# Kernel tuning notes

Hardware: AMD Instinct MI355X
Metric: run time of the kernel (lower is better)

Reference implementation:

```python
import jax, jax.numpy as jnp
import numpy as np

HEADS = 4
KDIM = 512
HALF = KDIM // 2
KNN = 16
NKEYS = 512
INPUT_DIM = 1024
VDIM = 512
B, T = 2, 1024


def setup_inputs() -> dict:
    key = jax.random.key(0)
    ks = jax.random.split(key, 5)
    bound_k = 1.0 / np.sqrt(KDIM)
    x = jax.random.normal(ks[0], (B, T, INPUT_DIM), dtype=jnp.float32)
    Wq = jax.random.normal(ks[1], (HEADS * KDIM, INPUT_DIM), dtype=jnp.float32) * (1.0 / np.sqrt(INPUT_DIM))
    bq = jnp.zeros((HEADS * KDIM,), dtype=jnp.float32)
    keys = jax.random.uniform(ks[2], (2 * HEADS * NKEYS, HALF), dtype=jnp.float32, minval=-bound_k, maxval=bound_k)
    values = jax.random.normal(ks[3], (NKEYS * NKEYS, VDIM), dtype=jnp.float32) * (VDIM ** -0.5)
    return {"x": x, "Wq": Wq, "bq": bq, "keys": keys, "values": values}


def reference(x, Wq, bq, keys, values):
    Bb, Tt, C = x.shape
    bs = Bb * Tt
    x_flat = x.reshape(bs, C)
    # query projection -> (bs, heads, k_dim)
    q = (x_flat @ Wq.T + bq).reshape(bs, HEADS, KDIM)
    q1, q2 = q[..., :HALF], q[..., HALF:]
    kk = keys.reshape(HEADS, 2, NKEYS, HALF)
    k1, k2 = kk[:, 0], kk[:, 1]
    # subspace scores: (bs, heads, n_keys)
    s1 = jnp.einsum('blh,lkh->blk', q1, k1)
    s2 = jnp.einsum('blh,lkh->blk', q2, k2)
    s1, i1 = jax.lax.top_k(s1, KNN)
    s2, i2 = jax.lax.top_k(s2, KNN)
    # cartesian merge -> (bs, heads, knn*knn)
    all_s = (s1[:, :, :, None] + s2[:, :, None, :]).reshape(bs, HEADS, KNN * KNN)
    all_i = (i1[:, :, :, None] * NKEYS + i2[:, :, None, :]).reshape(bs, HEADS, KNN * KNN)
    s, best = jax.lax.top_k(all_s, KNN)
    idx = jnp.take_along_axis(all_i, best, axis=2)  # (bs, heads, knn)
    # softmax per (token, head) over knn, in fp32 (matches torch F.softmax on (bs*heads, knn))
    w = jax.nn.softmax(s.astype(jnp.float32), axis=-1)
    idx_f = idx.reshape(bs, HEADS * KNN)
    w_f = w.reshape(bs, HEADS * KNN)
    # embedding_bag mode='sum' with per-sample weights
    out = jnp.einsum('bk,bkd->bd', w_f, values[idx_f].astype(jnp.float32))
    return out.reshape(Bb, Tt, VDIM).astype(x.dtype)
```

## Files before the change

kernel.cpp:

```cpp
#include <hip/hip_runtime.h>

typedef __attribute__((ext_vector_type(8))) _Float16 half8;
typedef __attribute__((ext_vector_type(8)))  short   short8;
typedef __attribute__((ext_vector_type(4)))  float   floatx4;
typedef __attribute__((ext_vector_type(2)))  float   floatx2;
typedef unsigned short ushort;

__device__ __forceinline__ void gl_lds16(const void* g, void* lds) {
    __builtin_amdgcn_global_load_lds(
        (const __attribute__((address_space(1))) unsigned int*)g,
        (__attribute__((address_space(3))) unsigned int*)lds,
        16, 0, 0);
}

__global__ void split2_kernel(const float* __restrict__ src,
                              _Float16* __restrict__ ph,
                              _Float16* __restrict__ pl, int n8) {
    int i = blockIdx.x * 256 + threadIdx.x;
    if (i >= n8) return;
    const float* s = src + (size_t)i * 8;
    floatx4 a = *(const floatx4*)s;
    floatx4 b = *(const floatx4*)(s + 4);
    float x[8];
    #pragma unroll
    for (int j = 0; j < 4; ++j) { x[j] = a[j]; x[j + 4] = b[j]; }
    half8 vh, vl;
    #pragma unroll
    for (int j = 0; j < 8; ++j) {
        _Float16 h = (_Float16)x[j];
        _Float16 l = (_Float16)((x[j] - (float)h) * 4096.0f);
        vh[j] = h; vl[j] = l;
    }
    *(half8*)(ph + (size_t)i * 8) = vh;
    *(half8*)(pl + (size_t)i * 8) = vl;
}

#define BM 128
#define BN 64
#define BK 32

template<int MODE>
__global__ __launch_bounds__(256) void gemm2_kernel(
    const _Float16* __restrict__ Ah, const _Float16* __restrict__ Al, int lda,
    const _Float16* __restrict__ Bh, const _Float16* __restrict__ Bl, int ldb,
    int K, const float* __restrict__ bias,
    float* __restrict__ C1, float* __restrict__ C2,
    _Float16* __restrict__ Qh, _Float16* __restrict__ Ql, int ldc)
{
    __shared__ _Float16 As[2][BM][BK];
    __shared__ _Float16 Bs[2][BN][BK];

    const int tid  = threadIdx.x;
    const int lane = tid & 63;
    const int w    = tid >> 6;
    const int wr   = w >> 1;
    const int wc   = w & 1;

    const size_t aRow = (size_t)blockIdx.y * BM;
    const size_t bRow = (size_t)blockIdx.x * BN;
    const _Float16 *Ah_p = Ah, *Al_p = Al, *Bh_p = Bh, *Bl_p = Bl;
    float* Cout = C1;
    if (MODE == 1) {
        int z = blockIdx.z;
        int h = z >> 1, c = z & 1;
        size_t aoff = (size_t)h * 512 + (size_t)c * 256;
        Ah_p += aoff; Al_p += aoff;
        size_t boff = (size_t)z * 512 * (size_t)ldb;
        Bh_p += boff; Bl_p += boff;
        Cout = (c ? C2 : C1) + (size_t)h * 512;
    }

    const int rr = lane >> 2;
    const int jj = (lane & 3) ^ ((lane >> 3) & 3);
    const size_t aStage = (aRow + rr) * (size_t)lda + jj * 8;
    const size_t bStage = (bRow + rr) * (size_t)ldb + jj * 8;

    const int rchunk = (lane >> 4) ^ ((lane >> 1) & 3);
    const int arow0  = wr * 64 + (lane & 15);
    const int brow0  = wc * 32 + (lane & 15);
    const _Float16* As0 = &As[0][0][0];
    const _Float16* Bs0 = &Bs[0][0][0];

    floatx4 acc0[4][2], acc1[4][2];
    #pragma unroll
    for (int m = 0; m < 4; ++m)
        #pragma unroll
        for (int n = 0; n < 2; ++n) { acc0[m][n] = (floatx4)0.0f; acc1[m][n] = (floatx4)0.0f; }

    for (int kt = 0; kt < K; kt += BK) {
        __syncthreads();
        for (int i = w; i < 24; i += 4) {
            if (i < 16) {
                int p = i >> 3, g = i & 7;
                const _Float16* base = p ? Al_p : Ah_p;
                gl_lds16(base + aStage + (size_t)(g * 16) * lda + kt,
                         (void*)(As0 + p * (BM * BK) + g * 16 * BK));
            } else {
                int p = (i >> 2) & 1, g = i & 3;
                const _Float16* base = p ? Bl_p : Bh_p;
                gl_lds16(base + bStage + (size_t)(g * 16) * ldb + kt,
                         (void*)(Bs0 + p * (BN * BK) + g * 16 * BK));
            }
        }
        __syncthreads();

        half8 a_h[4], a_l[4], b_h[2], b_l[2];
        #pragma unroll
        for (int m = 0; m < 4; ++m) {
            int off = (arow0 + m * 16) * BK + rchunk * 8;
            a_h[m] = *(const half8*)(As0 + off);
            a_l[m] = *(const half8*)(As0 + BM * BK + off);
        }
        #pragma unroll
        for (int n = 0; n < 2; ++n) {
            int off = (brow0 + n * 16) * BK + rchunk * 8;
            b_h[n] = *(const half8*)(Bs0 + off);
            b_l[n] = *(const half8*)(Bs0 + BN * BK + off);
        }
        #pragma unroll
        for (int m = 0; m < 4; ++m)
            #pragma unroll
            for (int n = 0; n < 2; ++n) {
                acc0[m][n] = __builtin_amdgcn_mfma_f32_16x16x32_f16(a_h[m], b_h[n], acc0[m][n], 0, 0, 0);
                acc1[m][n] = __builtin_amdgcn_mfma_f32_16x16x32_f16(a_h[m], b_l[n], acc1[m][n], 0, 0, 0);
                acc1[m][n] = __builtin_amdgcn_mfma_f32_16x16x32_f16(a_l[m], b_h[n], acc1[m][n], 0, 0, 0);
            }
    }

    #pragma unroll
    for (int m = 0; m < 4; ++m)
        #pragma unroll
        for (int n = 0; n < 2; ++n)
            #pragma unroll
            for (int r = 0; r < 4; ++r) {
                size_t row = aRow + wr * 64 + m * 16 + (lane >> 4) * 4 + r;
                size_t col = bRow + wc * 32 + n * 16 + (lane & 15);
                float v = acc0[m][n][r] + acc1[m][n][r] * (1.0f / 4096.0f);
                if (MODE == 0) {
                    v += bias[col];
                    _Float16 h = (_Float16)v;
                    _Float16 l = (_Float16)((v - (float)h) * 4096.0f);
                    Qh[row * ldc + col] = h;
                    Ql[row * ldc + col] = l;
                } else {
                    Cout[row * ldc + col] = v;
                }
            }
}

template<int L>
__device__ __forceinline__ void wave_topk16_reg(float (&v)[L], int lane,
                                                float (&selv)[16], int (&seli)[16]) {
    #pragma unroll
    for (int s = 0; s < 16; ++s) {
        float bv = v[0]; int bj = 0;
        #pragma unroll
        for (int j = 1; j < L; ++j) if (v[j] > bv) { bv = v[j]; bj = j; }
        int bi = lane * L + bj;
        #pragma unroll
        for (int off = 32; off > 0; off >>= 1) {
            float ov = __shfl_xor(bv, off, 64);
            int   oi = __shfl_xor(bi, off, 64);
            if (ov > bv || (ov == bv && oi < bi)) { bv = ov; bi = oi; }
        }
        selv[s] = bv; seli[s] = bi;
        int lj = bi - lane * L;
        #pragma unroll
        for (int j = 0; j < L; ++j) if (j == lj) v[j] = -3.4e38f;
    }
}

__global__ __launch_bounds__(256) void topk_gather_kernel(
    const float* __restrict__ s1, const float* __restrict__ s2,
    const float* __restrict__ values, float* __restrict__ out)
{
    __shared__ float sa[4][16];  __shared__ int ia_sh[4][16];
    __shared__ float sb[4][16];  __shared__ int ib_sh[4][16];
    __shared__ float wgt[4][16]; __shared__ int vidx[4][16];

    const int t = blockIdx.x, tid = threadIdx.x;
    const int h = tid >> 6, lane = tid & 63;

    const float* r1 = s1 + ((size_t)t * 4 + h) * 512;
    const float* r2 = s2 + ((size_t)t * 4 + h) * 512;
    float v1[8], v2[8];
    {
        floatx4 a0 = *(const floatx4*)(r1 + lane * 8);
        floatx4 a1 = *(const floatx4*)(r1 + lane * 8 + 4);
        floatx4 b0 = *(const floatx4*)(r2 + lane * 8);
        floatx4 b1 = *(const floatx4*)(r2 + lane * 8 + 4);
        #pragma unroll
        for (int j = 0; j < 4; ++j) { v1[j] = a0[j]; v1[j + 4] = a1[j]; v2[j] = b0[j]; v2[j + 4] = b1[j]; }
    }

    float selv1[16]; int seli1[16];
    wave_topk16_reg<8>(v1, lane, selv1, seli1);
    float selv2[16]; int seli2[16];
    wave_topk16_reg<8>(v2, lane, selv2, seli2);

    if (lane == 0) {
        #pragma unroll
        for (int s = 0; s < 16; ++s) {
            sa[h][s] = selv1[s]; ia_sh[h][s] = seli1[s];
            sb[h][s] = selv2[s]; ib_sh[h][s] = seli2[s];
        }
    }
    __syncthreads();

    float cv[4];
    #pragma unroll
    for (int cc = 0; cc < 4; ++cc) {
        int id = lane * 4 + cc;
        cv[cc] = sa[h][id >> 4] + sb[h][id & 15];
    }
    float fs[16]; int fid[16];
    wave_topk16_reg<4>(cv, lane, fs, fid);

    if (lane == 0) {
        float m = fs[0], sum = 0.f, e[16];
        #pragma unroll
        for (int s = 0; s < 16; ++s) { e[s] = expf(fs[s] - m); sum += e[s]; }
        float inv = 1.f / sum;
        #pragma unroll
        for (int s = 0; s < 16; ++s) {
            int id = fid[s];
            wgt[h][s]  = e[s] * inv;
            vidx[h][s] = ia_sh[h][id >> 4] * 512 + ib_sh[h][id & 15];
        }
    }
    __syncthreads();

    const int col = tid * 2;
    float ax = 0.f, ay = 0.f;
    #pragma unroll 4
    for (int e2 = 0; e2 < 64; ++e2) {
        int hh = e2 >> 4, k = e2 & 15;
        float wv = wgt[hh][k];
        int   id = vidx[hh][k];
        floatx2 v = *(const floatx2*)(values + (size_t)id * 512 + col);
        ax += wv * v[0]; ay += wv * v[1];
    }
    floatx2 o; o[0] = ax; o[1] = ay;
    *(floatx2*)(out + (size_t)t * 512 + col) = o;
}

extern "C" void kernel_launch(void* const* d_in, const int* in_sizes, int n_in,
                              void* d_out, int out_size, void* d_ws, size_t ws_size,
                              hipStream_t stream) {
    (void)in_sizes; (void)n_in; (void)out_size; (void)ws_size;
    const float* x      = (const float*)d_in[0];
    const float* Wq     = (const float*)d_in[1];
    const float* bq     = (const float*)d_in[2];
    const float* keys   = (const float*)d_in[3];
    const float* values = (const float*)d_in[4];
    float* out = (float*)d_out;

    char* ws = (char*)d_ws;
    const size_t MB = 1024 * 1024;
    _Float16* xh = (_Float16*)(ws + 0 * MB);
    _Float16* xl = (_Float16*)(ws + 4 * MB);
    _Float16* wh = (_Float16*)(ws + 8 * MB);
    _Float16* wl = (_Float16*)(ws + 12 * MB);
    _Float16* kh = (_Float16*)(ws + 16 * MB);
    _Float16* kl = (_Float16*)(ws + 18 * MB);
    _Float16* qh = (_Float16*)(ws + 20 * MB);
    _Float16* ql = (_Float16*)(ws + 28 * MB);
    float*    s1 = (float*)(ws + 36 * MB);
    float*    s2 = (float*)(ws + 52 * MB);

    split2_kernel<<<1024, 256, 0, stream>>>(x,    xh, xl, 262144);
    split2_kernel<<<1024, 256, 0, stream>>>(Wq,   wh, wl, 262144);
    split2_kernel<<<512,  256, 0, stream>>>(keys, kh, kl, 131072);

    gemm2_kernel<0><<<dim3(2048 / BN, 2048 / BM, 1), 256, 0, stream>>>(
        xh, xl, 1024, wh, wl, 1024, 1024, bq,
        nullptr, nullptr, qh, ql, 2048);

    gemm2_kernel<1><<<dim3(512 / BN, 2048 / BM, 8), 256, 0, stream>>>(
        qh, ql, 2048, kh, kl, 256, 256, nullptr,
        s1, s2, nullptr, nullptr, 2048);

    topk_gather_kernel<<<2048, 256, 0, stream>>>(s1, s2, values, out);
}
```

Baseline: 218.3 us.

## Double-buffer LDS tiles in split-fp16 GEMM to overlap loads with MFMA

Adds a second LDS buffer for the A/B hi/lo tiles and issues the global-to-LDS loads for the next K tile before computing on the current one. This lets memory latency overlap with MFMA work and cuts the per-iteration barriers from two to one. In exchange it doubles LDS usage per block, which may lower occupancy. It also relies on the single barrier at the end of each iteration to make both the prefetched data and the buffer reuse safe.

```diff
diff --git a/kernel.cpp b/kernel.cpp
--- a/kernel.cpp
+++ b/kernel.cpp
@@ -1,7 +1,6 @@
 #include <hip/hip_runtime.h>
 
 typedef __attribute__((ext_vector_type(8))) _Float16 half8;
-typedef __attribute__((ext_vector_type(8)))  short   short8;
 typedef __attribute__((ext_vector_type(4)))  float   floatx4;
 typedef __attribute__((ext_vector_type(2)))  float   floatx2;
 typedef unsigned short ushort;
@@ -47,8 +46,8 @@
     float* __restrict__ C1, float* __restrict__ C2,
     _Float16* __restrict__ Qh, _Float16* __restrict__ Ql, int ldc)
 {
-    __shared__ _Float16 As[2][BM][BK];
-    __shared__ _Float16 Bs[2][BN][BK];
+    __shared__ _Float16 As[2][2][BM][BK];
+    __shared__ _Float16 Bs[2][2][BN][BK];
 
     const int tid  = threadIdx.x;
     const int lane = tid & 63;
@@ -78,8 +77,25 @@
     const int rchunk = (lane >> 4) ^ ((lane >> 1) & 3);
     const int arow0  = wr * 64 + (lane & 15);
     const int brow0  = wc * 32 + (lane & 15);
-    const _Float16* As0 = &As[0][0][0];
-    const _Float16* Bs0 = &Bs[0][0][0];
+
+#define STAGE(buf, ktoff)                                                      \
+    {                                                                          \
+        _Float16* As0s = &As[buf][0][0][0];                                    \
+        _Float16* Bs0s = &Bs[buf][0][0][0];                                    \
+        for (int i = w; i < 24; i += 4) {                                      \
+            if (i < 16) {                                                      \
+                int p = i >> 3, g = i & 7;                                     \
+                const _Float16* base = p ? Al_p : Ah_p;                        \
+                gl_lds16(base + aStage + (size_t)(g * 16) * lda + (ktoff),     \
+                         (void*)(As0s + p * (BM * BK) + g * 16 * BK));         \
+            } else {                                                           \
+                int p = (i >> 2) & 1, g = i & 3;                               \
+                const _Float16* base = p ? Bl_p : Bh_p;                        \
+                gl_lds16(base + bStage + (size_t)(g * 16) * ldb + (ktoff),     \
+                         (void*)(Bs0s + p * (BN * BK) + g * 16 * BK));         \
+            }                                                                  \
+        }                                                                      \
+    }
 
     floatx4 acc0[4][2], acc1[4][2];
     #pragma unroll
@@ -87,23 +103,17 @@
         #pragma unroll
         for (int n = 0; n < 2; ++n) { acc0[m][n] = (floatx4)0.0f; acc1[m][n] = (floatx4)0.0f; }
 
-    for (int kt = 0; kt < K; kt += BK) {
-        __syncthreads();
-        for (int i = w; i < 24; i += 4) {
-            if (i < 16) {
-                int p = i >> 3, g = i & 7;
-                const _Float16* base = p ? Al_p : Ah_p;
-                gl_lds16(base + aStage + (size_t)(g * 16) * lda + kt,
-                         (void*)(As0 + p * (BM * BK) + g * 16 * BK));
-            } else {
-                int p = (i >> 2) & 1, g = i & 3;
-                const _Float16* base = p ? Bl_p : Bh_p;
-                gl_lds16(base + bStage + (size_t)(g * 16) * ldb + kt,
-                         (void*)(Bs0 + p * (BN * BK) + g * 16 * BK));
-            }
-        }
-        __syncthreads();
-
+    const int NT = K / BK;
+
+    STAGE(0, 0);
+    __syncthreads();
+
+    int cur = 0;
+    for (int t = 0; t < NT; ++t) {
+        if (t + 1 < NT) STAGE(cur ^ 1, (t + 1) * BK);
+
+        const _Float16* As0 = &As[cur][0][0][0];
+        const _Float16* Bs0 = &Bs[cur][0][0][0];
         half8 a_h[4], a_l[4], b_h[2], b_l[2];
         #pragma unroll
         for (int m = 0; m < 4; ++m) {
@@ -125,7 +135,11 @@
                 acc1[m][n] = __builtin_amdgcn_mfma_f32_16x16x32_f16(a_h[m], b_l[n], acc1[m][n], 0, 0, 0);
                 acc1[m][n] = __builtin_amdgcn_mfma_f32_16x16x32_f16(a_l[m], b_h[n], acc1[m][n], 0, 0, 0);
             }
-    }
+
+        __syncthreads();
+        cur ^= 1;
+    }
+#undef STAGE
 
     #pragma unroll
     for (int m = 0; m < 4; ++m)
```

New measurement: 214.9 us. Within noise of the previous version (-1.6%).
